# Optimization experiments

Hardware: AMD Instinct MI355X
Metric: run time of the kernel (lower is better)

Reference implementation:

```python
import jax, jax.numpy as jnp
import numpy as np

N = 50000   # nodes
E = 800000  # edges
D = 128     # hidden_dim == input_dim
H = 8       # heads
C = D // H  # per-head dim = 16
ED = 10     # edge_dim
FF = 4 * D  # ffn hidden = 512


def setup_inputs() -> dict:
    key = jax.random.key(0)
    ks = jax.random.split(key, 20)
    s = 0.05
    p = lambda k, shape: (jax.random.normal(k, shape, jnp.float32) * s)
    return {
        "x": jax.random.normal(ks[0], (N, D), jnp.float32),
        "edge_index": jax.random.randint(ks[1], (2, E), 0, N),
        "edge_attr": jax.random.normal(ks[2], (E, ED), jnp.float32),
        # TransformerConv params (PyG): lin_query/key/value have bias, lin_edge no bias,
        # lin_skip has bias, lin_beta no bias
        "Wq": p(ks[3], (D, D)), "bq": jnp.zeros((D,), jnp.float32),
        "Wk": p(ks[4], (D, D)), "bk": jnp.zeros((D,), jnp.float32),
        "Wv": p(ks[5], (D, D)), "bv": jnp.zeros((D,), jnp.float32),
        "We": p(ks[6], (ED, D)),
        "Wskip": p(ks[7], (D, D)), "bskip": jnp.zeros((D,), jnp.float32),
        "Wbeta": p(ks[8], (3 * D, 1)),
        # GraphNorm params
        "gn_w": jnp.ones((D,), jnp.float32),
        "gn_b": jnp.zeros((D,), jnp.float32),
        "gn_ms": jnp.ones((D,), jnp.float32),  # mean_scale
        # FFN params
        "W1": p(ks[9], (D, FF)), "b1": jnp.zeros((FF,), jnp.float32),
        "W2": p(ks[10], (FF, D)), "b2": jnp.zeros((D,), jnp.float32),
    }


def _layer(x, edge_index, edge_attr, Wq, bq, Wk, bk, Wv, bv, We, Wskip, bskip,
           Wbeta, gn_w, gn_b, gn_ms, W1, b1, W2, b2):
    n = x.shape[0]
    src, dst = edge_index[0], edge_index[1]
    # ---- TransformerConv (concat heads, edge-conditioned, beta skip) ----
    q = (x @ Wq + bq).reshape(n, H, C)
    k = (x @ Wk + bk).reshape(n, H, C)
    v = (x @ Wv + bv).reshape(n, H, C)
    e = (edge_attr @ We).reshape(-1, H, C)          # [E,H,C]
    k_j = k[src] + e                                 # gather + edge bias
    alpha = jnp.einsum('ehc,ehc->eh', q[dst], k_j) / jnp.sqrt(jnp.float32(C))
    # segment softmax over incoming edges of each target node
    amax = jax.ops.segment_max(alpha, dst, num_segments=n)      # [N,H]
    ex = jnp.exp(alpha - amax[dst])
    denom = jax.ops.segment_sum(ex, dst, num_segments=n)        # [N,H]
    alpha = ex / (denom[dst] + 1e-16)
    msg = (v[src] + e) * alpha[:, :, None]           # [E,H,C]
    out = jax.ops.segment_sum(msg.reshape(-1, H * C), dst, num_segments=n)  # [N,D]
    # beta-gated root skip
    x_r = x @ Wskip + bskip
    beta = jax.nn.sigmoid(jnp.concatenate([out, x_r, out - x_r], axis=-1) @ Wbeta)
    x_att = beta * x_r + (1.0 - beta) * out
    # ---- residual + GraphNorm (single graph) ----
    h = x + x_att
    mean = h.mean(axis=0)
    hc = h - gn_ms * mean
    var = (hc * hc).mean(axis=0)
    h = hc / jnp.sqrt(var + 1e-5) * gn_w + gn_b
    # ---- FFN with residual (GELU exact, matching torch default) ----
    ffn = jax.nn.gelu(h @ W1 + b1, approximate=False) @ W2 + b2
    return h + ffn


def reference(x, edge_index, edge_attr, Wq, bq, Wk, bk, Wv, bv, We, Wskip,
              bskip, Wbeta, gn_w, gn_b, gn_ms, W1, b1, W2, b2):
    return _layer(x, edge_index, edge_attr, Wq, bq, Wk, bk, Wv, bv, We, Wskip,
                  bskip, Wbeta, gn_w, gn_b, gn_ms, W1, b1, W2, b2)
```

## Files before the change

### kernel.cpp

```cpp
#include <hip/hip_runtime.h>
#include <hip/hip_fp16.h>
#include <math.h>

#define D 128
#define ED 10
#define FF 512
#define TPAD 520
#define XPAD 136

typedef __attribute__((ext_vector_type(4))) float f32x4;
typedef __attribute__((ext_vector_type(8))) short bf16x8;
using h2 = decltype(__builtin_amdgcn_cvt_pkrtz(0.f, 0.f));
typedef __attribute__((ext_vector_type(2))) float f32x2;

__device__ __forceinline__ ushort f2bf(float f) {
  unsigned u = __float_as_uint(f);
  unsigned r = u + 0x7fffu + ((u >> 16) & 1u);
  return (ushort)(r >> 16);
}
__device__ __forceinline__ float bf2f(ushort u) {
  return __uint_as_float(((unsigned)u) << 16);
}

#if __has_builtin(__builtin_amdgcn_cvt_pk_f32_fp8) && __has_builtin(__builtin_amdgcn_cvt_pk_fp8_f32)
#define FP8_HW 1
#else
#define FP8_HW 0
#endif

__device__ __forceinline__ unsigned sw_f2fp8(float f) {
  unsigned u = __float_as_uint(f);
  unsigned s = (u >> 24) & 0x80;
  int e = (int)((u >> 23) & 0xff) - 127;
  unsigned mant = u & 0x7fffff;
  if (e < -9) return s;
  if (e > 8) return s | 0x7e;
  if (e >= -6) {
    unsigned m = mant + 0x7ffff + ((mant >> 20) & 1);
    if (m >= 0x800000) { m = 0; ++e; if (e > 8) return s | 0x7e; }
    return s | ((unsigned)(e + 7) << 3) | (m >> 20);
  }
  unsigned full = 0x800000 | mant;
  int shift = 20 + (-6 - e);
  unsigned m = (full + (1u << (shift - 1)) + ((full >> shift) & 1)) >> shift;
  if (m >= 8) return s | 0x08;
  return s | m;
}
__device__ __forceinline__ float sw_fp82f(unsigned b) {
  unsigned s = (b & 0x80) << 24;
  unsigned e = (b >> 3) & 0xf;
  unsigned m = b & 7;
  if (e == 0) {
    if (m == 0) return __uint_as_float(s);
    float v = (float)(int)m * 0.001953125f;
    return (b & 0x80) ? -v : v;
  }
  return __uint_as_float(s | ((e + 120) << 23) | (m << 20));
}

__device__ __forceinline__ ushort pack_fp8_pair(float a, float b) {
#if FP8_HW
  int r = __builtin_amdgcn_cvt_pk_fp8_f32(a, b, 0, false);
  return (ushort)(r & 0xffff);
#else
  return (ushort)(sw_f2fp8(a) | (sw_f2fp8(b) << 8));
#endif
}
template <bool HI>
__device__ __forceinline__ f32x2 unpack_fp8_pair(unsigned w) {
#if FP8_HW
  auto r = __builtin_amdgcn_cvt_pk_f32_fp8((int)w, HI);
  f32x2 o; o[0] = r[0]; o[1] = r[1];
  return o;
#else
  unsigned v = HI ? (w >> 16) : w;
  f32x2 o; o[0] = sw_fp82f(v & 0xff); o[1] = sw_fp82f((v >> 8) & 0xff);
  return o;
#endif
}

__global__ void prep_hist(const float* __restrict__ Wq, const float* __restrict__ Wk,
                          const float* __restrict__ Wv, const float* __restrict__ Wskip,
                          const float* __restrict__ bq, const float* __restrict__ bk,
                          const float* __restrict__ bv, const float* __restrict__ bskip,
                          const float* __restrict__ W1, const float* __restrict__ W2,
                          const int* __restrict__ dst, int* __restrict__ deg,
                          int* __restrict__ rank, int E,
                          ushort* __restrict__ Wcat_t, float* __restrict__ bcat,
                          ushort* __restrict__ W1t, ushort* __restrict__ W2t) {
  int b = blockIdx.x;
  if (b >= 256) {
    int t = (b - 256) * 256 + threadIdx.x;
    if (t < E) rank[t] = atomicAdd(&deg[dst[t]], 1);
    return;
  }
  int t = b * 256 + threadIdx.x;
  {
    int w = t >> 14, c = (t >> 7) & 127, kk = t & 127;
    const float* W = (w == 0) ? Wq : (w == 1) ? Wk : (w == 2) ? Wv : Wskip;
    Wcat_t[t] = f2bf(W[kk * D + c]);
  }
  {
    int f = t >> 7, kk = t & 127;
    W1t[t] = f2bf(W1[kk * FF + f]);
  }
  {
    int c = t >> 9, f = t & 511;
    W2t[t] = f2bf(W2[f * D + c]);
  }
  if (t < 4 * D) {
    int w = t >> 7;
    const float* bb = (w == 0) ? bq : (w == 1) ? bk : (w == 2) ? bv : bskip;
    bcat[t] = bb[t & 127];
  }
}

__global__ __launch_bounds__(1024) void scan_kernel(const int* __restrict__ deg,
                                                    int* __restrict__ off, int n) {
  __shared__ int part[1024];
  int t = threadIdx.x;
  int chunk = (n + 1023) / 1024;
  int lo = t * chunk, hi = min(lo + chunk, n);
  int s = 0;
  for (int i = lo; i < hi; ++i) s += deg[i];
  part[t] = s;
  __syncthreads();
  for (int dd = 1; dd < 1024; dd <<= 1) {
    int v = (t >= dd) ? part[t - dd] : 0;
    __syncthreads();
    part[t] += v;
    __syncthreads();
  }
  int excl = (t == 0) ? 0 : part[t - 1];
  for (int i = lo; i < hi; ++i) {
    off[i] = excl;
    excl += deg[i];
  }
  if (t == 1023) off[n] = part[1023];
}

__global__ void scatter_kernel(const int* __restrict__ dst, const int* __restrict__ rank,
                               const int* __restrict__ off, int* __restrict__ sorted, int E) {
  int t = blockIdx.x * blockDim.x + threadIdx.x;
  if (t >= E) return;
  sorted[off[dst[t]] + rank[t]] = t;
}

__global__ __launch_bounds__(256) void gemm_in(
    const float* __restrict__ x, const ushort* __restrict__ Wcat_t,
    const float* __restrict__ bcat, ushort* __restrict__ qb, unsigned* __restrict__ kvf8,
    float* __restrict__ xr, int n) {
  __shared__ ushort xa[32 * XPAD];
  int r0 = blockIdx.x * 32;
  {
    int row = threadIdx.x >> 3;
    int seg = threadIdx.x & 7;
    int grow = min(r0 + row, n - 1);
    const float4* p = reinterpret_cast<const float4*>(x + (size_t)grow * D + seg * 16);
    float4 f0 = p[0], f1 = p[1], f2 = p[2], f3 = p[3];
    bf16x8 u0, u1;
    u0[0] = (short)f2bf(f0.x); u0[1] = (short)f2bf(f0.y);
    u0[2] = (short)f2bf(f0.z); u0[3] = (short)f2bf(f0.w);
    u0[4] = (short)f2bf(f1.x); u0[5] = (short)f2bf(f1.y);
    u0[6] = (short)f2bf(f1.z); u0[7] = (short)f2bf(f1.w);
    u1[0] = (short)f2bf(f2.x); u1[1] = (short)f2bf(f2.y);
    u1[2] = (short)f2bf(f2.z); u1[3] = (short)f2bf(f2.w);
    u1[4] = (short)f2bf(f3.x); u1[5] = (short)f2bf(f3.y);
    u1[6] = (short)f2bf(f3.z); u1[7] = (short)f2bf(f3.w);
    ushort* dl = xa + row * XPAD + seg * 16;
    *reinterpret_cast<bf16x8*>(dl) = u0;
    *reinterpret_cast<bf16x8*>(dl + 8) = u1;
  }
  __syncthreads();
  int wv = threadIdx.x >> 6;
  int l = threadIdx.x & 63;
  int lr = l & 15, lg = l >> 4;
  const ushort* Wt = Wcat_t + wv * D * D;
  f32x4 acc[2][8];
#pragma unroll
  for (int m = 0; m < 2; ++m)
#pragma unroll
    for (int nn = 0; nn < 8; ++nn) acc[m][nn] = (f32x4)0.f;
#pragma unroll
  for (int kb2 = 0; kb2 < 4; ++kb2) {
    int k0 = kb2 * 32 + lg * 8;
    bf16x8 a[2];
#pragma unroll
    for (int m = 0; m < 2; ++m)
      a[m] = *reinterpret_cast<const bf16x8*>(xa + (m * 16 + lr) * XPAD + k0);
    bf16x8 b[8];
#pragma unroll
    for (int nn = 0; nn < 8; ++nn)
      b[nn] = *reinterpret_cast<const bf16x8*>(Wt + (nn * 16 + lr) * D + k0);
#pragma unroll
    for (int m = 0; m < 2; ++m)
#pragma unroll
      for (int nn = 0; nn < 8; ++nn)
        acc[m][nn] = __builtin_amdgcn_mfma_f32_16x16x32_bf16(a[m], b[nn], acc[m][nn], 0, 0, 0);
  }
#pragma unroll
  for (int m = 0; m < 2; ++m)
#pragma unroll
    for (int nn = 0; nn < 8; ++nn) {
      int col = nn * 16 + lr;
      float bb = bcat[wv * D + col];
#pragma unroll
      for (int j = 0; j < 4; ++j) {
        int row = r0 + m * 16 + lg * 4 + j;
        float val = acc[m][nn][j] + bb;
        if (wv == 1 || wv == 2) {
          float partner = __shfl_xor(val, 1, 64);
          if (((lr & 1) == 0) && row < n) {
            ushort us = pack_fp8_pair(val, partner);
            size_t idx = ((size_t)row * 64 + nn * 8 + (lr >> 1)) * 2 + (wv - 1);
            reinterpret_cast<ushort*>(kvf8)[idx] = us;
          }
        } else if (row < n) {
          if (wv == 0) qb[(size_t)row * D + col] = f2bf(val);
          else xr[(size_t)row * D + col] = val;
        }
      }
    }
}

__global__ __launch_bounds__(256) void node_attn(
    const int* __restrict__ src, const int* __restrict__ sorted,
    const int* __restrict__ off, const float* __restrict__ attr,
    const float* __restrict__ We, const ushort* __restrict__ qb,
    const unsigned* __restrict__ kvf8, const float* __restrict__ xr,
    const float* __restrict__ x, const float* __restrict__ Wbeta,
    float* __restrict__ h, float* __restrict__ sums, int n) {
  __shared__ h2 attrS[4][64][5];
  __shared__ float rs_h[4 * D], rs_h2[4 * D];
  int wid = threadIdx.x >> 6;
  int l = threadIdx.x & 63;
  int d0 = 2 * l;
  h2 wA[5], wB[5];
#pragma unroll
  for (int t = 0; t < 5; ++t) {
    wA[t] = __builtin_amdgcn_cvt_pkrtz(We[(2 * t) * D + d0], We[(2 * t + 1) * D + d0]);
    wB[t] = __builtin_amdgcn_cvt_pkrtz(We[(2 * t) * D + d0 + 1], We[(2 * t + 1) * D + d0 + 1]);
  }
  float2 wb0 = *reinterpret_cast<const float2*>(Wbeta + d0);
  float2 wb1 = *reinterpret_cast<const float2*>(Wbeta + D + d0);
  float2 wb2 = *reinterpret_cast<const float2*>(Wbeta + 2 * D + d0);
  float s_h0 = 0.f, s_h20 = 0.f, s_h1 = 0.f, s_h21 = 0.f;
  for (int node = blockIdx.x * 4 + wid; node < n; node += gridDim.x * 4) {
    const ushort2 qu = *reinterpret_cast<const ushort2*>(qb + (size_t)node * D + d0);
    float q0 = bf2f(qu.x) * 0.25f, q1 = bf2f(qu.y) * 0.25f;
    int o0 = off[node], dg = off[node + 1] - o0;
    float m = -1e30f, den = 0.f, acc0 = 0.f, acc1 = 0.f;
    for (int chunk = 0; chunk < dg; chunk += 64) {
      int cnt = min(64, dg - chunk);
      int s_l = 0;
      {
        int e_l = 0;
        if (chunk + l < dg) {
          e_l = sorted[o0 + chunk + l];
          s_l = src[e_l];
        }
        const float2* ap = reinterpret_cast<const float2*>(attr + (size_t)e_l * ED);
#pragma unroll
        for (int j = 0; j < 5; ++j) {
          float2 av = ap[j];
          attrS[wid][l][j] = __builtin_amdgcn_cvt_pkrtz(av.x, av.y);
        }
      }
      auto LD = [&](int idx) -> unsigned {
        int ss = __shfl(s_l, min(idx, cnt - 1));
        return kvf8[(size_t)ss * 64 + l];
      };
      auto PROC = [&](unsigned kvw, int i) {
        h2 a0 = attrS[wid][i][0], a1 = attrS[wid][i][1], a2 = attrS[wid][i][2],
           a3 = attrS[wid][i][3], a4 = attrS[wid][i][4];
        float ec0 = __builtin_amdgcn_fdot2(a0, wA[0], 0.f, false);
        ec0 = __builtin_amdgcn_fdot2(a1, wA[1], ec0, false);
        ec0 = __builtin_amdgcn_fdot2(a2, wA[2], ec0, false);
        ec0 = __builtin_amdgcn_fdot2(a3, wA[3], ec0, false);
        ec0 = __builtin_amdgcn_fdot2(a4, wA[4], ec0, false);
        float ec1 = __builtin_amdgcn_fdot2(a0, wB[0], 0.f, false);
        ec1 = __builtin_amdgcn_fdot2(a1, wB[1], ec1, false);
        ec1 = __builtin_amdgcn_fdot2(a2, wB[2], ec1, false);
        ec1 = __builtin_amdgcn_fdot2(a3, wB[3], ec1, false);
        ec1 = __builtin_amdgcn_fdot2(a4, wB[4], ec1, false);
        f32x2 kf = unpack_fp8_pair<false>(kvw);
        f32x2 vf = unpack_fp8_pair<true>(kvw);
        float kk0 = kf[0] + ec0, kk1 = kf[1] + ec1;
        float vv0 = vf[0] + ec0, vv1 = vf[1] + ec1;
        float p = fmaf(q0, kk0, q1 * kk1);
        p += __shfl_xor(p, 1, 8);
        p += __shfl_xor(p, 2, 8);
        p += __shfl_xor(p, 4, 8);
        if (__any(p > m + 8.f)) {
          float mn = fmaxf(m, p);
          float sc = __expf(m - mn);
          den *= sc; acc0 *= sc; acc1 *= sc;
          m = mn;
        }
        float ex = __expf(p - m);
        den += ex;
        acc0 = fmaf(ex, vv0, acc0);
        acc1 = fmaf(ex, vv1, acc1);
      };
      unsigned kv0 = LD(0), kv1 = LD(1), kv2 = LD(2), kv3 = LD(3);
      for (int i = 0; i < cnt; i += 4) {
        unsigned c0 = kv0, c1 = kv1, c2 = kv2, c3 = kv3;
        kv0 = LD(i + 4); kv1 = LD(i + 5); kv2 = LD(i + 6); kv3 = LD(i + 7);
        PROC(c0, i);
        if (i + 1 < cnt) PROC(c1, i + 1);
        if (i + 2 < cnt) PROC(c2, i + 2);
        if (i + 3 < cnt) PROC(c3, i + 3);
      }
    }
    float inv = 1.f / (den + 1e-16f);
    float oo0 = acc0 * inv, oo1 = acc1 * inv;
    float2 xr2 = *reinterpret_cast<const float2*>(xr + (size_t)node * D + d0);
    float2 x2 = *reinterpret_cast<const float2*>(x + (size_t)node * D + d0);
    float pb = oo0 * wb0.x + xr2.x * wb1.x + (oo0 - xr2.x) * wb2.x
             + oo1 * wb0.y + xr2.y * wb1.y + (oo1 - xr2.y) * wb2.y;
#pragma unroll
    for (int msk = 1; msk < 64; msk <<= 1) pb += __shfl_xor(pb, msk, 64);
    float beta = 1.f / (1.f + __expf(-pb));
    float h0 = x2.x + beta * xr2.x + (1.f - beta) * oo0;
    float h1 = x2.y + beta * xr2.y + (1.f - beta) * oo1;
    *reinterpret_cast<float2*>(h + (size_t)node * D + d0) = make_float2(h0, h1);
    s_h0 += h0; s_h20 += h0 * h0;
    s_h1 += h1; s_h21 += h1 * h1;
  }
  rs_h[wid * D + d0] = s_h0;   rs_h[wid * D + d0 + 1] = s_h1;
  rs_h2[wid * D + d0] = s_h20; rs_h2[wid * D + d0 + 1] = s_h21;
  __syncthreads();
  if (threadIdx.x < D) {
    int d = threadIdx.x;
    float sh = rs_h[d] + rs_h[D + d] + rs_h[2 * D + d] + rs_h[3 * D + d];
    float sh2 = rs_h2[d] + rs_h2[D + d] + rs_h2[2 * D + d] + rs_h2[3 * D + d];
    atomicAdd(&sums[d], sh);
    atomicAdd(&sums[D + d], sh2);
  }
}

__global__ __launch_bounds__(256) void ffn_fused(
    const float* __restrict__ h, const float* __restrict__ sums,
    const float* __restrict__ gn_w, const float* __restrict__ gn_b,
    const float* __restrict__ gn_ms,
    const ushort* __restrict__ W1t, const float* __restrict__ b1,
    const ushort* __restrict__ W2t, const float* __restrict__ b2,
    float* __restrict__ out, float inv_n, int n) {
  __shared__ ushort xa[32 * XPAD];
  __shared__ ushort tt[32 * TPAD];
  __shared__ float scsh[2 * D];
  if (threadIdx.x < D) {
    int d = threadIdx.x;
    float mean = sums[d] * inv_n;
    float ex2 = sums[D + d] * inv_n;
    float ms = gn_ms[d];
    float var = ex2 - 2.f * ms * mean * mean + ms * ms * mean * mean;
    float inv = 1.f / sqrtf(var + 1e-5f);
    float scale = gn_w[d] * inv;
    scsh[d] = scale;
    scsh[D + d] = gn_b[d] - ms * mean * scale;
  }
  __syncthreads();
  int r0 = blockIdx.x * 32;
  {
    int row = threadIdx.x >> 3;
    int seg = threadIdx.x & 7;
    int grow = min(r0 + row, n - 1);
    const float4* p = reinterpret_cast<const float4*>(h + (size_t)grow * D + seg * 16);
    float4 f0 = p[0], f1 = p[1], f2 = p[2], f3 = p[3];
    const float4* sc = reinterpret_cast<const float4*>(scsh + seg * 16);
    const float4* sh = reinterpret_cast<const float4*>(scsh + D + seg * 16);
    float4 s0 = sc[0], s1 = sc[1], s2 = sc[2], s3 = sc[3];
    float4 t0 = sh[0], t1 = sh[1], t2 = sh[2], t3 = sh[3];
    bf16x8 u0, u1;
    u0[0] = (short)f2bf(f0.x * s0.x + t0.x); u0[1] = (short)f2bf(f0.y * s0.y + t0.y);
    u0[2] = (short)f2bf(f0.z * s0.z + t0.z); u0[3] = (short)f2bf(f0.w * s0.w + t0.w);
    u0[4] = (short)f2bf(f1.x * s1.x + t1.x); u0[5] = (short)f2bf(f1.y * s1.y + t1.y);
    u0[6] = (short)f2bf(f1.z * s1.z + t1.z); u0[7] = (short)f2bf(f1.w * s1.w + t1.w);
    u1[0] = (short)f2bf(f2.x * s2.x + t2.x); u1[1] = (short)f2bf(f2.y * s2.y + t2.y);
    u1[2] = (short)f2bf(f2.z * s2.z + t2.z); u1[3] = (short)f2bf(f2.w * s2.w + t2.w);
    u1[4] = (short)f2bf(f3.x * s3.x + t3.x); u1[5] = (short)f2bf(f3.y * s3.y + t3.y);
    u1[6] = (short)f2bf(f3.z * s3.z + t3.z); u1[7] = (short)f2bf(f3.w * s3.w + t3.w);
    ushort* dl = xa + row * XPAD + seg * 16;
    *reinterpret_cast<bf16x8*>(dl) = u0;
    *reinterpret_cast<bf16x8*>(dl + 8) = u1;
  }
  __syncthreads();
  int wv = threadIdx.x >> 6;
  int l = threadIdx.x & 63;
  int lr = l & 15, lg = l >> 4;
  int c0 = wv * 128;
  {
    f32x4 acc[2][8];
#pragma unroll
    for (int m = 0; m < 2; ++m)
#pragma unroll
      for (int nn = 0; nn < 8; ++nn) acc[m][nn] = (f32x4)0.f;
#pragma unroll
    for (int kb = 0; kb < 4; ++kb) {
      int k0 = kb * 32 + lg * 8;
      bf16x8 a[2];
#pragma unroll
      for (int m = 0; m < 2; ++m)
        a[m] = *reinterpret_cast<const bf16x8*>(xa + (m * 16 + lr) * XPAD + k0);
      bf16x8 b[8];
#pragma unroll
      for (int nn = 0; nn < 8; ++nn)
        b[nn] = *reinterpret_cast<const bf16x8*>(W1t + (c0 + nn * 16 + lr) * D + k0);
#pragma unroll
      for (int m = 0; m < 2; ++m)
#pragma unroll
        for (int nn = 0; nn < 8; ++nn)
          acc[m][nn] = __builtin_amdgcn_mfma_f32_16x16x32_bf16(a[m], b[nn], acc[m][nn], 0, 0, 0);
    }
    const float inv_sqrt2 = 0.70710678118654752440f;
#pragma unroll
    for (int m = 0; m < 2; ++m)
#pragma unroll
      for (int nn = 0; nn < 8; ++nn) {
        int col = c0 + nn * 16 + lr;
        float bb = b1[col];
#pragma unroll
        for (int j = 0; j < 4; ++j) {
          int rowl = m * 16 + lg * 4 + j;
          float val = acc[m][nn][j] + bb;
          val = 0.5f * val * (1.f + erff(val * inv_sqrt2));
          tt[rowl * TPAD + col] = f2bf(val);
        }
      }
  }
  __syncthreads();
  {
    f32x4 acc[2][2];
#pragma unroll
    for (int m = 0; m < 2; ++m)
#pragma unroll
      for (int nn = 0; nn < 2; ++nn) acc[m][nn] = (f32x4)0.f;
#pragma unroll 4
    for (int kb = 0; kb < 16; ++kb) {
      int k0 = kb * 32 + lg * 8;
      bf16x8 a[2];
#pragma unroll
      for (int m = 0; m < 2; ++m)
        a[m] = *reinterpret_cast<const bf16x8*>(tt + (m * 16 + lr) * TPAD + k0);
      bf16x8 b[2];
#pragma unroll
      for (int nn = 0; nn < 2; ++nn)
        b[nn] = *reinterpret_cast<const bf16x8*>(W2t + (wv * 32 + nn * 16 + lr) * FF + k0);
#pragma unroll
      for (int m = 0; m < 2; ++m)
#pragma unroll
        for (int nn = 0; nn < 2; ++nn)
          acc[m][nn] = __builtin_amdgcn_mfma_f32_16x16x32_bf16(a[m], b[nn], acc[m][nn], 0, 0, 0);
    }
#pragma unroll
    for (int m = 0; m < 2; ++m)
#pragma unroll
      for (int nn = 0; nn < 2; ++nn) {
        int col = wv * 32 + nn * 16 + lr;
        float bb = b2[col];
#pragma unroll
        for (int j = 0; j < 4; ++j) {
          int rowl = m * 16 + lg * 4 + j;
          int row = r0 + rowl;
          if (row < n) {
            float hn = bf2f(xa[rowl * XPAD + col]);
            out[(size_t)row * D + col] = hn + acc[m][nn][j] + bb;
          }
        }
      }
  }
}

extern "C" void kernel_launch(void* const* d_in, const int* in_sizes, int n_in,
                              void* d_out, int out_size, void* d_ws, size_t ws_size,
                              hipStream_t stream) {
  const float* x     = (const float*)d_in[0];
  const int*   ei    = (const int*)d_in[1];
  const float* attr  = (const float*)d_in[2];
  const float* Wq    = (const float*)d_in[3];
  const float* bq    = (const float*)d_in[4];
  const float* Wk    = (const float*)d_in[5];
  const float* bk    = (const float*)d_in[6];
  const float* Wv    = (const float*)d_in[7];
  const float* bv    = (const float*)d_in[8];
  const float* We    = (const float*)d_in[9];
  const float* Wskip = (const float*)d_in[10];
  const float* bskip = (const float*)d_in[11];
  const float* Wbeta = (const float*)d_in[12];
  const float* gn_w  = (const float*)d_in[13];
  const float* gn_b  = (const float*)d_in[14];
  const float* gn_ms = (const float*)d_in[15];
  const float* W1    = (const float*)d_in[16];
  const float* b1    = (const float*)d_in[17];
  const float* W2    = (const float*)d_in[18];
  const float* b2    = (const float*)d_in[19];

  const int n = in_sizes[0] / D;
  const int E = in_sizes[1] / 2;
  const int* src = ei;
  const int* dst = ei + E;
  const size_t ND = (size_t)n * D;

  ushort* qb = (ushort*)d_ws;
  unsigned* kvf8 = (unsigned*)(qb + ND);
  float* xr = (float*)(kvf8 + (size_t)n * 64);
  int* deg = (int*)(xr + ND);
  float* sums = (float*)(deg + n);
  int* off = (int*)(sums + 2 * D);
  int* sorted = off + n + 1;
  int* rank = sorted + E;
  ushort* Wcat_t = (ushort*)(rank + E);
  ushort* W1t = Wcat_t + 4 * D * D;
  ushort* W2t = W1t + D * FF;
  float* bcat = (float*)(W2t + FF * D);

  (void)hipMemsetAsync(deg, 0, ((size_t)n + 2 * D) * sizeof(int), stream);

  int ghist = (E + 255) / 256;
  prep_hist<<<256 + ghist, 256, 0, stream>>>(Wq, Wk, Wv, Wskip, bq, bk, bv, bskip, W1, W2,
                                             dst, deg, rank, E, Wcat_t, bcat, W1t, W2t);
  scan_kernel<<<1, 1024, 0, stream>>>(deg, off, n);
  scatter_kernel<<<ghist, 256, 0, stream>>>(dst, rank, off, sorted, E);

  gemm_in<<<(n + 31) / 32, 256, 0, stream>>>(x, Wcat_t, bcat, qb, kvf8, xr, n);

  node_attn<<<2048, 256, 0, stream>>>(src, sorted, off, attr, We, qb, kvf8, xr, x, Wbeta,
                                      (float*)d_out, sums, n);

  ffn_fused<<<(n + 31) / 32, 256, 0, stream>>>((const float*)d_out, sums, gn_w, gn_b, gn_ms,
                                               W1t, b1, W2t, b2, (float*)d_out,
                                               1.f / (float)n, n);
}
```

Measured before the change: 399.7 us.

## Pre-permute src and fp16 edge attrs in scatter; deepen kv prefetch to 8

The scatter kernel now writes the source index and fp16-packed edge attributes directly into dst-sorted order, so the attention kernel reads them contiguously instead of through a double indirection (sorted then src/attr). This removes random gathers from the hot attention loop and halves attribute bytes there, in exchange for an extra scattered write pass of E*20 bytes in the scatter kernel. The attention loop also prefetches 8 kv words instead of 4 to hide gather latency, at the cost of more registers.

```diff
diff --git a/kernel.cpp b/kernel.cpp
--- a/kernel.cpp
+++ b/kernel.cpp
@@ -139,11 +139,21 @@
   if (t == 1023) off[n] = part[1023];
 }
 
-__global__ void scatter_kernel(const int* __restrict__ dst, const int* __restrict__ rank,
-                               const int* __restrict__ off, int* __restrict__ sorted, int E) {
+__global__ void scatter_kernel(const int* __restrict__ dst, const int* __restrict__ src,
+                               const int* __restrict__ rank, const int* __restrict__ off,
+                               const float* __restrict__ attr, int* __restrict__ srcs,
+                               unsigned* __restrict__ attrh, int E) {
   int t = blockIdx.x * blockDim.x + threadIdx.x;
   if (t >= E) return;
-  sorted[off[dst[t]] + rank[t]] = t;
+  int pos = off[dst[t]] + rank[t];
+  srcs[pos] = src[t];
+  const float2* ap = reinterpret_cast<const float2*>(attr + (size_t)t * ED);
+#pragma unroll
+  for (int j = 0; j < 5; ++j) {
+    float2 av = ap[j];
+    h2 hh = __builtin_amdgcn_cvt_pkrtz(av.x, av.y);
+    attrh[(size_t)pos * 5 + j] = __builtin_bit_cast(unsigned, hh);
+  }
 }
 
 __global__ __launch_bounds__(256) void gemm_in(
@@ -224,13 +234,13 @@
 }
 
 __global__ __launch_bounds__(256) void node_attn(
-    const int* __restrict__ src, const int* __restrict__ sorted,
-    const int* __restrict__ off, const float* __restrict__ attr,
-    const float* __restrict__ We, const ushort* __restrict__ qb,
-    const unsigned* __restrict__ kvf8, const float* __restrict__ xr,
-    const float* __restrict__ x, const float* __restrict__ Wbeta,
-    float* __restrict__ h, float* __restrict__ sums, int n) {
-  __shared__ h2 attrS[4][64][5];
+    const int* __restrict__ srcs, const int* __restrict__ off,
+    const unsigned* __restrict__ attrh, const float* __restrict__ We,
+    const ushort* __restrict__ qb, const unsigned* __restrict__ kvf8,
+    const float* __restrict__ xr, const float* __restrict__ x,
+    const float* __restrict__ Wbeta, float* __restrict__ h,
+    float* __restrict__ sums, int n) {
+  __shared__ unsigned attrS[4][64][5];
   __shared__ float rs_h[4 * D], rs_h2[4 * D];
   int wid = threadIdx.x >> 6;
   int l = threadIdx.x & 63;
@@ -253,26 +263,23 @@
     for (int chunk = 0; chunk < dg; chunk += 64) {
       int cnt = min(64, dg - chunk);
       int s_l = 0;
-      {
-        int e_l = 0;
-        if (chunk + l < dg) {
-          e_l = sorted[o0 + chunk + l];
-          s_l = src[e_l];
-        }
-        const float2* ap = reinterpret_cast<const float2*>(attr + (size_t)e_l * ED);
-#pragma unroll
-        for (int j = 0; j < 5; ++j) {
-          float2 av = ap[j];
-          attrS[wid][l][j] = __builtin_amdgcn_cvt_pkrtz(av.x, av.y);
-        }
+      if (l < cnt) {
+        size_t pos = (size_t)(o0 + chunk + l);
+        s_l = srcs[pos];
+        const unsigned* ah = attrh + pos * 5;
+#pragma unroll
+        for (int j = 0; j < 5; ++j) attrS[wid][l][j] = ah[j];
       }
       auto LD = [&](int idx) -> unsigned {
         int ss = __shfl(s_l, min(idx, cnt - 1));
         return kvf8[(size_t)ss * 64 + l];
       };
       auto PROC = [&](unsigned kvw, int i) {
-        h2 a0 = attrS[wid][i][0], a1 = attrS[wid][i][1], a2 = attrS[wid][i][2],
-           a3 = attrS[wid][i][3], a4 = attrS[wid][i][4];
+        h2 a0 = __builtin_bit_cast(h2, attrS[wid][i][0]);
+        h2 a1 = __builtin_bit_cast(h2, attrS[wid][i][1]);
+        h2 a2 = __builtin_bit_cast(h2, attrS[wid][i][2]);
+        h2 a3 = __builtin_bit_cast(h2, attrS[wid][i][3]);
+        h2 a4 = __builtin_bit_cast(h2, attrS[wid][i][4]);
         float ec0 = __builtin_amdgcn_fdot2(a0, wA[0], 0.f, false);
         ec0 = __builtin_amdgcn_fdot2(a1, wA[1], ec0, false);
         ec0 = __builtin_amdgcn_fdot2(a2, wA[2], ec0, false);
@@ -302,14 +309,20 @@
         acc0 = fmaf(ex, vv0, acc0);
         acc1 = fmaf(ex, vv1, acc1);
       };
-      unsigned kv0 = LD(0), kv1 = LD(1), kv2 = LD(2), kv3 = LD(3);
-      for (int i = 0; i < cnt; i += 4) {
-        unsigned c0 = kv0, c1 = kv1, c2 = kv2, c3 = kv3;
-        kv0 = LD(i + 4); kv1 = LD(i + 5); kv2 = LD(i + 6); kv3 = LD(i + 7);
+      unsigned p0 = LD(0), p1 = LD(1), p2 = LD(2), p3 = LD(3),
+               p4 = LD(4), p5 = LD(5), p6 = LD(6), p7 = LD(7);
+      for (int i = 0; i < cnt; i += 8) {
+        unsigned c0 = p0, c1 = p1, c2 = p2, c3 = p3, c4 = p4, c5 = p5, c6 = p6, c7 = p7;
+        p0 = LD(i + 8);  p1 = LD(i + 9);  p2 = LD(i + 10); p3 = LD(i + 11);
+        p4 = LD(i + 12); p5 = LD(i + 13); p6 = LD(i + 14); p7 = LD(i + 15);
         PROC(c0, i);
         if (i + 1 < cnt) PROC(c1, i + 1);
         if (i + 2 < cnt) PROC(c2, i + 2);
         if (i + 3 < cnt) PROC(c3, i + 3);
+        if (i + 4 < cnt) PROC(c4, i + 4);
+        if (i + 5 < cnt) PROC(c5, i + 5);
+        if (i + 6 < cnt) PROC(c6, i + 6);
+        if (i + 7 < cnt) PROC(c7, i + 7);
       }
     }
     float inv = 1.f / (den + 1e-16f);
@@ -508,9 +521,10 @@
   int* deg = (int*)(xr + ND);
   float* sums = (float*)(deg + n);
   int* off = (int*)(sums + 2 * D);
-  int* sorted = off + n + 1;
-  int* rank = sorted + E;
-  ushort* Wcat_t = (ushort*)(rank + E);
+  int* srcs = off + n + 1;
+  int* rank = srcs + E;
+  unsigned* attrh = (unsigned*)(rank + E);
+  ushort* Wcat_t = (ushort*)(attrh + (size_t)E * 5);
   ushort* W1t = Wcat_t + 4 * D * D;
   ushort* W2t = W1t + D * FF;
   float* bcat = (float*)(W2t + FF * D);
@@ -521,11 +535,11 @@
   prep_hist<<<256 + ghist, 256, 0, stream>>>(Wq, Wk, Wv, Wskip, bq, bk, bv, bskip, W1, W2,
                                              dst, deg, rank, E, Wcat_t, bcat, W1t, W2t);
   scan_kernel<<<1, 1024, 0, stream>>>(deg, off, n);
-  scatter_kernel<<<ghist, 256, 0, stream>>>(dst, rank, off, sorted, E);
+  scatter_kernel<<<ghist, 256, 0, stream>>>(dst, src, rank, off, attr, srcs, attrh, E);
 
   gemm_in<<<(n + 31) / 32, 256, 0, stream>>>(x, Wcat_t, bcat, qb, kvf8, xr, n);
 
-  node_attn<<<2048, 256, 0, stream>>>(src, sorted, off, attr, We, qb, kvf8, xr, x, Wbeta,
+  node_attn<<<2048, 256, 0, stream>>>(srcs, off, attrh, We, qb, kvf8, xr, x, Wbeta,
                                       (float*)d_out, sums, n);
 
   ffn_fused<<<(n + 31) / 32, 256, 0, stream>>>((const float*)d_out, sums, gn_w, gn_b, gn_ms,
```

Result: slower. 416.2 us (+4.1%).
